# Kernel optimization log

Hardware: AMD Instinct MI355X
Metric: run time of the kernel (lower is better)

## Reference

```python
import jax, jax.numpy as jnp
import numpy as np

N_EMBD = 1024
HEAD_SIZE = 64


def setup_inputs() -> dict:
    key = jax.random.key(0)
    k1, k2, k3, k4 = jax.random.split(key, 4)
    x = jax.random.normal(k1, (8, 2048, N_EMBD), dtype=jnp.float32)
    # torch Linear(n_embd, head_size, bias=False): y = x @ W.T with W [out,in].
    # Store as [in, out] so y = x @ W. Scale init like torch default (~1/sqrt(in)).
    s = 1.0 / np.sqrt(N_EMBD)
    Wk = jax.random.uniform(k2, (N_EMBD, HEAD_SIZE), jnp.float32, -s, s)
    Wq = jax.random.uniform(k3, (N_EMBD, HEAD_SIZE), jnp.float32, -s, s)
    Wv = jax.random.uniform(k4, (N_EMBD, HEAD_SIZE), jnp.float32, -s, s)
    return {"x": x, "Wk": Wk, "Wq": Wq, "Wv": Wv}


def reference(x, Wk, Wq, Wv):
    # x: [B,T,C]
    B, T, C = x.shape
    k = x @ Wk  # [B,T,H]
    q = x @ Wq  # [B,T,H]
    v = x @ Wv  # [B,T,H]
    scale = HEAD_SIZE ** -0.5
    wei = jnp.einsum('bth,bsh->bts', q, k) * scale  # [B,T,T]
    causal = jnp.tril(jnp.ones((T, T), dtype=bool))  # [T,T]
    wei = jnp.where(causal[None, :, :], wei, -jnp.inf)
    wei = jax.nn.softmax(wei, axis=-1)
    # dropout(p=0.2) is identity in eval mode (deterministic baseline)
    out = jnp.einsum('bts,bsh->bth', wei, v)  # [B,T,H]
    return out
```

## Files before the change

### kernel.cpp

```cpp
#include <hip/hip_runtime.h>
#include <hip/hip_bf16.h>

#define B_DIM 8
#define T_DIM 2048
#define C_DIM 1024
#define H_DIM 64
#define BT (B_DIM * T_DIM)

typedef __attribute__((ext_vector_type(8))) short bf16x8;
typedef __attribute__((ext_vector_type(4))) float f32x4;

__device__ __forceinline__ ushort f2bf(float f) {
    __hip_bfloat16 h = __float2bfloat16(f);
    return *reinterpret_cast<ushort*>(&h);
}
__device__ __forceinline__ unsigned int packbf(float a, float b) {
    return (unsigned int)f2bf(a) | ((unsigned int)f2bf(b) << 16);
}

__global__ __launch_bounds__(256) void wt_convert_kernel(
    const float* __restrict__ Wk, const float* __restrict__ Wq,
    const float* __restrict__ Wv, ushort* __restrict__ wt)
{
    const int n = blockIdx.x;
    const float* src = (n < 64) ? Wk : (n < 128) ? Wq : Wv;
    const float scale = (n >= 64 && n < 128) ? 0.125f * 1.4426950408889634f : 1.0f;
    const int col = n & 63;
    for (int k = threadIdx.x; k < C_DIM; k += 256)
        wt[(size_t)n * C_DIM + k] = f2bf(src[(size_t)k * H_DIM + col] * scale);
}

__global__ __launch_bounds__(256) void qkv_gemm_kernel(
    const float* __restrict__ x, const ushort* __restrict__ wt,
    ushort* __restrict__ kb, ushort* __restrict__ qb, ushort* __restrict__ vt)
{
    __shared__ ushort Xf[2][4 * 64 * 8];
    const int tid = threadIdx.x;
    const int wave = tid >> 6, lane = tid & 63;
    const int col = lane & 15, quad = lane >> 4;
    const int r0 = blockIdx.x * 32;

    f32x4 acc[2][3];
    #pragma unroll
    for (int m = 0; m < 2; ++m)
        #pragma unroll
        for (int i = 0; i < 3; ++i) acc[m][i] = (f32x4){0.f, 0.f, 0.f, 0.f};

    const int xrow = (wave >> 1) * 16 + col;
    const int xcc  = (wave & 1) * 4 + quad;
    const float* xsrc = x + (size_t)(r0 + xrow) * C_DIM + xcc * 8;

    const ushort* wsrc[3][2];
    #pragma unroll
    for (int j = 0; j < 3; ++j)
        #pragma unroll
        for (int ks = 0; ks < 2; ++ks)
            wsrc[j][ks] = wt + (size_t)((wave * 3 + j) * 16 + col) * C_DIM
                             + ks * 32 + quad * 8;

    {
        const float4 f0 = *(const float4*)(xsrc);
        const float4 f1 = *(const float4*)(xsrc + 4);
        uint4 u;
        u.x = packbf(f0.x, f0.y); u.y = packbf(f0.z, f0.w);
        u.z = packbf(f1.x, f1.y); u.w = packbf(f1.z, f1.w);
        *(uint4*)&Xf[0][(wave * 64 + lane) * 8] = u;
    }
    bf16x8 wcur[3][2];
    #pragma unroll
    for (int j = 0; j < 3; ++j)
        #pragma unroll
        for (int ks = 0; ks < 2; ++ks)
            wcur[j][ks] = *(const bf16x8*)(wsrc[j][ks]);
    __syncthreads();

    for (int i = 0; i < 16; ++i) {
        const int b = i & 1;
        bf16x8 wnxt[3][2];
        float4 nf0, nf1;
        if (i < 15) {
            const int k1 = (i + 1) * 64;
            #pragma unroll
            for (int j = 0; j < 3; ++j)
                #pragma unroll
                for (int ks = 0; ks < 2; ++ks)
                    wnxt[j][ks] = *(const bf16x8*)(wsrc[j][ks] + k1);
            nf0 = *(const float4*)(xsrc + k1);
            nf1 = *(const float4*)(xsrc + k1 + 4);
        }
        #pragma unroll
        for (int ks = 0; ks < 2; ++ks) {
            const bf16x8 a0 = *(const bf16x8*)&Xf[b][((    ks) * 64 + lane) * 8];
            const bf16x8 a1 = *(const bf16x8*)&Xf[b][((2 + ks) * 64 + lane) * 8];
            #pragma unroll
            for (int j = 0; j < 3; ++j) {
                acc[0][j] = __builtin_amdgcn_mfma_f32_16x16x32_bf16(a0, wcur[j][ks], acc[0][j], 0, 0, 0);
                acc[1][j] = __builtin_amdgcn_mfma_f32_16x16x32_bf16(a1, wcur[j][ks], acc[1][j], 0, 0, 0);
            }
        }
        if (i < 15) {
            #pragma unroll
            for (int j = 0; j < 3; ++j)
                #pragma unroll
                for (int ks = 0; ks < 2; ++ks)
                    wcur[j][ks] = wnxt[j][ks];
            uint4 u;
            u.x = packbf(nf0.x, nf0.y); u.y = packbf(nf0.z, nf0.w);
            u.z = packbf(nf1.x, nf1.y); u.w = packbf(nf1.z, nf1.w);
            *(uint4*)&Xf[b ^ 1][(wave * 64 + lane) * 8] = u;
        }
        __syncthreads();
    }

    #pragma unroll
    for (int i = 0; i < 3; ++i) {
        const int nt = wave * 3 + i;
        #pragma unroll
        for (int mf = 0; mf < 2; ++mf) {
            const int rbase = r0 + mf * 16 + quad * 4;
            if (nt < 4) {
                const int n = nt * 16 + col;
                #pragma unroll
                for (int r = 0; r < 4; ++r)
                    kb[(size_t)(rbase + r) * H_DIM + n] = f2bf(acc[mf][i][r]);
            } else if (nt < 8) {
                const int n = nt * 16 + col - 64;
                #pragma unroll
                for (int r = 0; r < 4; ++r)
                    qb[(size_t)(rbase + r) * H_DIM + n] = f2bf(acc[mf][i][r]);
            } else {
                const int h = nt * 16 + col - 128;
                const int vbatch = rbase >> 11, vrow = rbase & (T_DIM - 1);
                ushort u4[4] = {f2bf(acc[mf][i][0]), f2bf(acc[mf][i][1]),
                                f2bf(acc[mf][i][2]), f2bf(acc[mf][i][3])};
                unsigned long long uu; __builtin_memcpy(&uu, u4, 8);
                *(unsigned long long*)(vt + ((size_t)vbatch * H_DIM + h) * T_DIM + vrow) = uu;
            }
        }
    }
}

__global__ __launch_bounds__(256) void attn_kernel(
    const ushort* __restrict__ kb, const ushort* __restrict__ qb,
    const ushort* __restrict__ vt, float* __restrict__ out)
{
    __shared__ unsigned int Ps[4][16 * 34];
    __shared__ float Om[4][64][17];
    __shared__ float Mm[4][16], Lm[4][16];

    const int tid = threadIdx.x;
    const int wave = tid >> 6, lane = tid & 63;
    const int col = lane & 15, quad = lane >> 4;
    const int batch = blockIdx.x & 7;
    const int qtile = 127 - (blockIdx.x >> 3);
    const int q0 = qtile * 16;

    const ushort* kbase = kb + (size_t)batch * T_DIM * H_DIM;
    const ushort* vbase = vt + (size_t)batch * H_DIM * T_DIM;

    const size_t qoff = (size_t)(batch * T_DIM + q0 + col) * H_DIM + quad * 8;
    const bf16x8 bq0 = *(const bf16x8*)(qb + qoff);
    const bf16x8 bq1 = *(const bf16x8*)(qb + qoff + 32);

    float m_ = -INFINITY, l_ = 0.f;
    f32x4 o_[4];
    #pragma unroll
    for (int i = 0; i < 4; ++i) o_[i] = (f32x4){0.f, 0.f, 0.f, 0.f};

    const int ntiles = (q0 + 16 + 63) >> 6;
    unsigned int* psw = &Ps[wave][0];

    for (int t = wave; t < ntiles; t += 4) {
        const int kb0 = t * 64;
        f32x4 s[4];
        #pragma unroll
        for (int mt = 0; mt < 4; ++mt) s[mt] = (f32x4){0.f, 0.f, 0.f, 0.f};
        #pragma unroll
        for (int ks = 0; ks < 2; ++ks) {
            const bf16x8 bq = ks ? bq1 : bq0;
            #pragma unroll
            for (int mt = 0; mt < 4; ++mt) {
                const bf16x8 ak = *(const bf16x8*)
                    (kbase + (size_t)(kb0 + mt * 16 + col) * H_DIM + ks * 32 + quad * 8);
                s[mt] = __builtin_amdgcn_mfma_f32_16x16x32_bf16(ak, bq, s[mt], 0, 0, 0);
            }
        }
        if (kb0 + 63 > q0) {
            const int kq = kb0 + quad * 4 - q0 - col;
            #pragma unroll
            for (int mt = 0; mt < 4; ++mt)
                #pragma unroll
                for (int reg = 0; reg < 4; ++reg)
                    if (kq + mt * 16 + reg > 0) s[mt][reg] = -INFINITY;
        }
        float mr = -INFINITY;
        #pragma unroll
        for (int mt = 0; mt < 4; ++mt)
            #pragma unroll
            for (int reg = 0; reg < 4; ++reg) mr = fmaxf(mr, s[mt][reg]);
        mr = fmaxf(mr, __shfl_xor(mr, 16));
        mr = fmaxf(mr, __shfl_xor(mr, 32));
        const float mn = fmaxf(m_, mr);
        const float corr = exp2f(m_ - mn);
        float sum = 0.f;
        #pragma unroll
        for (int mt = 0; mt < 4; ++mt)
            #pragma unroll
            for (int reg = 0; reg < 4; ++reg) {
                const float pv = exp2f(s[mt][reg] - mn);
                s[mt][reg] = pv;
                sum += pv;
            }
        sum += __shfl_xor(sum, 16);
        sum += __shfl_xor(sum, 32);
        l_ = l_ * corr + sum;
        m_ = mn;
        #pragma unroll
        for (int ht = 0; ht < 4; ++ht) o_[ht] *= corr;
        #pragma unroll
        for (int mt = 0; mt < 4; ++mt) {
            uint2 w2;
            w2.x = packbf(s[mt][0], s[mt][1]);
            w2.y = packbf(s[mt][2], s[mt][3]);
            *(uint2*)&psw[col * 34 + mt * 8 + quad * 2] = w2;
        }
        #pragma unroll
        for (int ks2 = 0; ks2 < 2; ++ks2) {
            const uint2 ra = *(const uint2*)&psw[col * 34 + ks2 * 16 + quad * 4];
            const uint2 rb = *(const uint2*)&psw[col * 34 + ks2 * 16 + quad * 4 + 2];
            unsigned int ub[4] = {ra.x, ra.y, rb.x, rb.y};
            bf16x8 bp; __builtin_memcpy(&bp, ub, 16);
            #pragma unroll
            for (int ht = 0; ht < 4; ++ht) {
                const bf16x8 av = *(const bf16x8*)
                    (vbase + (size_t)(ht * 16 + col) * T_DIM + kb0 + ks2 * 32 + quad * 8);
                o_[ht] = __builtin_amdgcn_mfma_f32_16x16x32_bf16(av, bp, o_[ht], 0, 0, 0);
            }
        }
    }

    #pragma unroll
    for (int ht = 0; ht < 4; ++ht)
        #pragma unroll
        for (int reg = 0; reg < 4; ++reg)
            Om[wave][ht * 16 + quad * 4 + reg][col] = o_[ht][reg];
    if (lane < 16) { Mm[wave][lane] = m_; Lm[wave][lane] = l_; }
    __syncthreads();
    {
        const int q = tid >> 4, hb = tid & 15;
        const float M = fmaxf(fmaxf(Mm[0][q], Mm[1][q]), fmaxf(Mm[2][q], Mm[3][q]));
        const float a0 = exp2f(Mm[0][q] - M), a1 = exp2f(Mm[1][q] - M);
        const float a2 = exp2f(Mm[2][q] - M), a3 = exp2f(Mm[3][q] - M);
        const float L = Lm[0][q] * a0 + Lm[1][q] * a1 + Lm[2][q] * a2 + Lm[3][q] * a3;
        const float rL = 1.0f / L;
        float* orow = out + (size_t)(batch * T_DIM + q0 + q) * H_DIM;
        #pragma unroll
        for (int i = 0; i < 4; ++i) {
            const int h = hb + 16 * i;
            orow[h] = (Om[0][h][q] * a0 + Om[1][h][q] * a1 +
                       Om[2][h][q] * a2 + Om[3][h][q] * a3) * rL;
        }
    }
}

extern "C" void kernel_launch(void* const* d_in, const int* in_sizes, int n_in,
                              void* d_out, int out_size, void* d_ws, size_t ws_size,
                              hipStream_t stream)
{
    const float* x  = (const float*)d_in[0];
    const float* Wk = (const float*)d_in[1];
    const float* Wq = (const float*)d_in[2];
    const float* Wv = (const float*)d_in[3];

    ushort* kbuf = (ushort*)d_ws;
    ushort* qbuf = kbuf + (size_t)BT * H_DIM;
    ushort* vtb  = qbuf + (size_t)BT * H_DIM;
    ushort* wt   = vtb  + (size_t)BT * H_DIM;

    wt_convert_kernel<<<192, 256, 0, stream>>>(Wk, Wq, Wv, wt);
    qkv_gemm_kernel<<<BT / 32, 256, 0, stream>>>(x, wt, kbuf, qbuf, vtb);
    attn_kernel<<<B_DIM * 128, 256, 0, stream>>>(kbuf, qbuf, vtb, (float*)d_out);
}
```

Before: 156.2 us.

## Lazy softmax rescale, fast exp2, MFMA priority hints, tiled weight transpose

The attention loop now rescales the running max and output accumulators only when some lane's row max exceeds the old max by more than 8 (log2 units), so most tiles skip the correction multiply. It also uses the hardware exp2 intrinsic, builds the max and sum as trees, and raises wave priority around the MFMA sections. The weight conversion kernel now transposes through a shared-memory tile with coalesced reads and vectorized writes. Lazy rescaling lets unnormalized exponentials grow up to 2^8, a small risk to bf16 precision. The raw exp2 intrinsic skips denormal handling.

```diff
diff --git a/kernel.cpp b/kernel.cpp
--- a/kernel.cpp
+++ b/kernel.cpp
@@ -22,12 +22,26 @@
     const float* __restrict__ Wk, const float* __restrict__ Wq,
     const float* __restrict__ Wv, ushort* __restrict__ wt)
 {
-    const int n = blockIdx.x;
-    const float* src = (n < 64) ? Wk : (n < 128) ? Wq : Wv;
-    const float scale = (n >= 64 && n < 128) ? 0.125f * 1.4426950408889634f : 1.0f;
-    const int col = n & 63;
-    for (int k = threadIdx.x; k < C_DIM; k += 256)
-        wt[(size_t)n * C_DIM + k] = f2bf(src[(size_t)k * H_DIM + col] * scale);
+    __shared__ float tile[64][65];
+    const int mat = blockIdx.x >> 4;
+    const int k0 = (blockIdx.x & 15) << 6;
+    const float* src = (mat == 0) ? Wk : (mat == 1) ? Wq : Wv;
+    const float scale = (mat == 1) ? 0.125f * 1.4426950408889634f : 1.0f;
+    #pragma unroll
+    for (int i = 0; i < 16; ++i) {
+        const int idx = i * 256 + threadIdx.x;
+        const int r = idx >> 6, c = idx & 63;
+        tile[r][c] = src[(size_t)(k0 + r) * H_DIM + c];
+    }
+    __syncthreads();
+    const int c = threadIdx.x >> 2, r0 = (threadIdx.x & 3) << 4;
+    unsigned int u[8];
+    #pragma unroll
+    for (int j = 0; j < 8; ++j)
+        u[j] = packbf(tile[r0 + 2 * j][c] * scale, tile[r0 + 2 * j + 1][c] * scale);
+    ushort* dst = wt + (size_t)(mat * 64 + c) * C_DIM + k0 + r0;
+    *(uint4*)(dst)     = (uint4){u[0], u[1], u[2], u[3]};
+    *(uint4*)(dst + 8) = (uint4){u[4], u[5], u[6], u[7]};
 }
 
 __global__ __launch_bounds__(256) void qkv_gemm_kernel(
@@ -175,6 +189,7 @@
         f32x4 s[4];
         #pragma unroll
         for (int mt = 0; mt < 4; ++mt) s[mt] = (f32x4){0.f, 0.f, 0.f, 0.f};
+        __builtin_amdgcn_s_setprio(1);
         #pragma unroll
         for (int ks = 0; ks < 2; ++ks) {
             const bf16x8 bq = ks ? bq1 : bq0;
@@ -185,6 +200,7 @@
                 s[mt] = __builtin_amdgcn_mfma_f32_16x16x32_bf16(ak, bq, s[mt], 0, 0, 0);
             }
         }
+        __builtin_amdgcn_s_setprio(0);
         if (kb0 + 63 > q0) {
             const int kq = kb0 + quad * 4 - q0 - col;
             #pragma unroll
@@ -193,30 +209,37 @@
                 for (int reg = 0; reg < 4; ++reg)
                     if (kq + mt * 16 + reg > 0) s[mt][reg] = -INFINITY;
         }
-        float mr = -INFINITY;
-        #pragma unroll
-        for (int mt = 0; mt < 4; ++mt)
-            #pragma unroll
-            for (int reg = 0; reg < 4; ++reg) mr = fmaxf(mr, s[mt][reg]);
+        float mr;
+        {
+            const float a = fmaxf(s[0][0], s[0][1]), b = fmaxf(s[0][2], s[0][3]);
+            const float c = fmaxf(s[1][0], s[1][1]), d = fmaxf(s[1][2], s[1][3]);
+            const float e = fmaxf(s[2][0], s[2][1]), f = fmaxf(s[2][2], s[2][3]);
+            const float g = fmaxf(s[3][0], s[3][1]), h = fmaxf(s[3][2], s[3][3]);
+            mr = fmaxf(fmaxf(fmaxf(a, b), fmaxf(c, d)),
+                       fmaxf(fmaxf(e, f), fmaxf(g, h)));
+        }
         mr = fmaxf(mr, __shfl_xor(mr, 16));
         mr = fmaxf(mr, __shfl_xor(mr, 32));
-        const float mn = fmaxf(m_, mr);
-        const float corr = exp2f(m_ - mn);
-        float sum = 0.f;
-        #pragma unroll
-        for (int mt = 0; mt < 4; ++mt)
-            #pragma unroll
-            for (int reg = 0; reg < 4; ++reg) {
-                const float pv = exp2f(s[mt][reg] - mn);
-                s[mt][reg] = pv;
-                sum += pv;
-            }
+        if (__any(mr > m_ + 8.f)) {
+            const float mn = fmaxf(m_, mr);
+            const float corr = __builtin_amdgcn_exp2f(m_ - mn);
+            l_ *= corr;
+            #pragma unroll
+            for (int ht = 0; ht < 4; ++ht) o_[ht] *= corr;
+            m_ = mn;
+        }
+        float psum[4];
+        #pragma unroll
+        for (int mt = 0; mt < 4; ++mt) {
+            #pragma unroll
+            for (int reg = 0; reg < 4; ++reg)
+                s[mt][reg] = __builtin_amdgcn_exp2f(s[mt][reg] - m_);
+            psum[mt] = (s[mt][0] + s[mt][1]) + (s[mt][2] + s[mt][3]);
+        }
+        float sum = (psum[0] + psum[1]) + (psum[2] + psum[3]);
         sum += __shfl_xor(sum, 16);
         sum += __shfl_xor(sum, 32);
-        l_ = l_ * corr + sum;
-        m_ = mn;
-        #pragma unroll
-        for (int ht = 0; ht < 4; ++ht) o_[ht] *= corr;
+        l_ += sum;
         #pragma unroll
         for (int mt = 0; mt < 4; ++mt) {
             uint2 w2;
@@ -224,6 +247,7 @@
             w2.y = packbf(s[mt][2], s[mt][3]);
             *(uint2*)&psw[col * 34 + mt * 8 + quad * 2] = w2;
         }
+        __builtin_amdgcn_s_setprio(1);
         #pragma unroll
         for (int ks2 = 0; ks2 < 2; ++ks2) {
             const uint2 ra = *(const uint2*)&psw[col * 34 + ks2 * 16 + quad * 4];
@@ -237,6 +261,7 @@
                 o_[ht] = __builtin_amdgcn_mfma_f32_16x16x32_bf16(av, bp, o_[ht], 0, 0, 0);
             }
         }
+        __builtin_amdgcn_s_setprio(0);
     }
 
     #pragma unroll
@@ -249,8 +274,10 @@
     {
         const int q = tid >> 4, hb = tid & 15;
         const float M = fmaxf(fmaxf(Mm[0][q], Mm[1][q]), fmaxf(Mm[2][q], Mm[3][q]));
-        const float a0 = exp2f(Mm[0][q] - M), a1 = exp2f(Mm[1][q] - M);
-        const float a2 = exp2f(Mm[2][q] - M), a3 = exp2f(Mm[3][q] - M);
+        const float a0 = __builtin_amdgcn_exp2f(Mm[0][q] - M);
+        const float a1 = __builtin_amdgcn_exp2f(Mm[1][q] - M);
+        const float a2 = __builtin_amdgcn_exp2f(Mm[2][q] - M);
+        const float a3 = __builtin_amdgcn_exp2f(Mm[3][q] - M);
         const float L = Lm[0][q] * a0 + Lm[1][q] * a1 + Lm[2][q] * a2 + Lm[3][q] * a3;
         const float rL = 1.0f / L;
         float* orow = out + (size_t)(batch * T_DIM + q0 + q) * H_DIM;
@@ -277,7 +304,7 @@
     ushort* vtb  = qbuf + (size_t)BT * H_DIM;
     ushort* wt   = vtb  + (size_t)BT * H_DIM;
 
-    wt_convert_kernel<<<192, 256, 0, stream>>>(Wk, Wq, Wv, wt);
+    wt_convert_kernel<<<48, 256, 0, stream>>>(Wk, Wq, Wv, wt);
     qkv_gemm_kernel<<<BT / 32, 256, 0, stream>>>(x, wt, kbuf, qbuf, vtb);
     attn_kernel<<<B_DIM * 128, 256, 0, stream>>>(kbuf, qbuf, vtb, (float*)d_out);
 }
```

New measurement: 159.2 us. No clear change (+2.0%).
